# Optimization experiments

Hardware: AMD Instinct MI355X
Metric: run time of the kernel (lower is better)

The kernel has to match this reference:

```python
import jax, jax.numpy as jnp
import numpy as np

N, E, H, C, G = 20000, 320000, 6, 64, 64
NFEAT, EDGE_DIM = 6, 1
HC = H * C  # 384


def gat_conv(x, src, dst, ea, W, a_src, a_dst, W_e, a_e, b):
    """PyG GATConv (concat=True, negative_slope=0.2), self-loops already added.
    x:[N,in], src/dst:[E'], ea:[E',edge_dim]. Returns [N,H*C]."""
    n = x.shape[0]
    h = (x @ W.T).reshape(n, H, C)                       # [N,H,C]
    a_s = (h * a_src).sum(-1)                            # [N,H]
    a_d = (h * a_dst).sum(-1)                            # [N,H]
    e = (ea @ W_e.T).reshape(-1, H, C)                   # [E',H,C]
    a_ed = (e * a_e).sum(-1)                             # [E',H]
    alpha = jax.nn.leaky_relu(a_s[src] + a_d[dst] + a_ed, 0.2)
    # segment softmax over incoming edges of each dst node (stable)
    m = jax.ops.segment_max(alpha, dst, num_segments=n)  # every node has a self-loop
    ex = jnp.exp(alpha - m[dst])
    den = jax.ops.segment_sum(ex, dst, num_segments=n)
    att = ex / den[dst]                                  # [E',H]
    msg = h[src] * att[:, :, None]                       # [E',H,C]
    out = jax.ops.segment_sum(msg, dst, num_segments=n)
    return out.reshape(n, HC) + b


def add_self_loops(edge_index, edge_attr, n):
    loops = jnp.arange(n, dtype=edge_index.dtype)
    src = jnp.concatenate([edge_index[0], loops])
    dst = jnp.concatenate([edge_index[1], loops])
    fill = jnp.broadcast_to(edge_attr.mean(0, keepdims=True), (n, edge_attr.shape[1]))
    ea = jnp.concatenate([edge_attr, fill], axis=0)
    return src, dst, ea


def setup_inputs() -> dict:
    key = jax.random.key(0)
    ks = jax.random.split(key, 20)
    glorot = lambda k, shape: jax.random.normal(k, shape, jnp.float32) * np.sqrt(2.0 / (shape[-1] + shape[0]))
    inp = {
        "x": jax.random.normal(ks[0], (N, NFEAT), jnp.float32),
        "edge_attr": jax.random.uniform(ks[1], (E, EDGE_DIM), jnp.float32),
        "edge_index": jax.random.randint(ks[2], (2, E), 0, N, jnp.int64),
        "batch": jnp.sort(jax.random.randint(ks[3], (N,), 0, G, jnp.int64)),
        # conv1 params
        "w1": glorot(ks[4], (HC, NFEAT)),
        "att_src1": glorot(ks[5], (1, H, C)),
        "att_dst1": glorot(ks[6], (1, H, C)),
        "we1": glorot(ks[7], (HC, EDGE_DIM)),
        "atte1": glorot(ks[8], (1, H, C)),
        "b1": jnp.zeros((HC,), jnp.float32),
        # conv2 params
        "w2": glorot(ks[9], (HC, HC)),
        "att_src2": glorot(ks[10], (1, H, C)),
        "att_dst2": glorot(ks[11], (1, H, C)),
        "we2": glorot(ks[12], (HC, EDGE_DIM)),
        "atte2": glorot(ks[13], (1, H, C)),
        "b2": jnp.zeros((HC,), jnp.float32),
        # final linear (no bias)
        "w_lin": glorot(ks[14], (1, HC)),
    }
    return inp


def reference(x, edge_attr, w1, att_src1, att_dst1, we1, atte1, b1,
              w2, att_src2, att_dst2, we2, atte2, b2, w_lin,
              edge_index, batch):
    src, dst, ea = add_self_loops(edge_index, edge_attr, N)
    x1 = gat_conv(x, src, dst, ea, w1, att_src1, att_dst1, we1, atte1, b1)
    x2 = jax.nn.elu(x1)
    x3 = gat_conv(x2, src, dst, ea, w2, att_src2, att_dst2, we2, atte2, b2)
    x4 = jax.nn.elu(x3)
    # global mean pool over graphs
    sums = jax.ops.segment_sum(x4, batch, num_segments=G)
    cnt = jax.ops.segment_sum(jnp.ones((N, 1), x4.dtype), batch, num_segments=G)
    x5 = sums / jnp.maximum(cnt, 1.0)
    # dropout is identity in eval mode
    x7 = x5 @ w_lin.T
    return jax.nn.sigmoid(x7)
```

## Files before the change

### kernel.cpp

```cpp
#include <hip/hip_runtime.h>
#include <hip/hip_bf16.h>

constexpr int Nn  = 20000;
constexpr int Ee  = 320000;
constexpr int Hh  = 6;
constexpr int HC  = 384;
constexpr int Gg  = 64;
constexpr int NF  = 6;
constexpr int EP  = Ee + Nn;
constexpr int HW  = HC / 2;

typedef __attribute__((ext_vector_type(8))) short short8;
typedef __attribute__((ext_vector_type(4))) float f32x4;

constexpr size_t ALN(size_t x) { return (x + 255) & ~(size_t)255; }
constexpr size_t OFF_H1BF = 0;
constexpr size_t OFF_X2BF = ALN(OFF_H1BF + (size_t)Nn*HW*4);
constexpr size_t OFF_ATT  = ALN(OFF_X2BF + (size_t)Nn*HW*4);
constexpr size_t OFF_AS1  = ALN(OFF_ATT  + (size_t)EP*Hh*4);
constexpr size_t OFF_AD1  = ALN(OFF_AS1  + (size_t)Nn*Hh*4);
constexpr size_t OFF_AS2  = ALN(OFF_AD1  + (size_t)Nn*Hh*4);
constexpr size_t OFF_AD2  = ALN(OFF_AS2  + (size_t)Nn*Hh*4);
constexpr size_t OFF_OFFS = ALN(OFF_AD2  + (size_t)Nn*Hh*4);
constexpr size_t OFF_ESRC = ALN(OFF_OFFS + (size_t)(Nn+1)*4);
constexpr size_t OFF_EEA  = ALN(OFF_ESRC + (size_t)EP*4);
constexpr size_t OFF_W2BF = ALN(OFF_EEA  + (size_t)EP*4);
constexpr size_t OFF_ZERO = ALN(OFF_W2BF + (size_t)HC*HC*2);
constexpr size_t OFF_CNT  = OFF_ZERO;
constexpr size_t OFF_CNT2 = OFF_CNT  + (size_t)Nn*4;
constexpr size_t OFF_CNTG = OFF_CNT2 + (size_t)Nn*4;
constexpr size_t OFF_POOL = OFF_CNTG + (size_t)Gg*4;
constexpr size_t OFF_SCAL = OFF_POOL + (size_t)Gg*HC*4;
constexpr size_t ZERO_BYTES = OFF_SCAL + 64*4 - OFF_ZERO;

__device__ __forceinline__ float wave_red64(float v) {
    #pragma unroll
    for (int o = 32; o; o >>= 1) v += __shfl_down(v, o);
    return v;
}
__device__ __forceinline__ unsigned short f2bf(float f) {
    union { float f; unsigned u; } v; v.f = f;
    return (unsigned short)((v.u + 0x7fffu + ((v.u >> 16) & 1u)) >> 16);
}
__device__ __forceinline__ unsigned pack2(float a, float b) {
    return (unsigned)f2bf(a) | ((unsigned)f2bf(b) << 16);
}
__device__ __forceinline__ float blo(unsigned w) { union { unsigned u; float f; } v; v.u = w << 16; return v.f; }
__device__ __forceinline__ float bhi(unsigned w) { union { unsigned u; float f; } v; v.u = w & 0xffff0000u; return v.f; }

__global__ void k_mean(const float* __restrict__ ea, float* __restrict__ scal) {
    int i = blockIdx.x * blockDim.x + threadIdx.x;
    float v = 0.f;
    for (int j = i; j < Ee; j += gridDim.x * blockDim.x) v += ea[j];
    v = wave_red64(v);
    if ((threadIdx.x & 63) == 0) atomicAdd(&scal[0], v);
}

__global__ void k_wedot(const float* __restrict__ we1, const float* __restrict__ atte1,
                        const float* __restrict__ we2, const float* __restrict__ atte2,
                        float* __restrict__ scal) {
    int t = threadIdx.x;
    float p1 = we1[t] * atte1[t];
    float p2 = we2[t] * atte2[t];
    p1 = wave_red64(p1);
    p2 = wave_red64(p2);
    if ((t & 63) == 0) { int h = t >> 6; scal[1 + h] = p1; scal[7 + h] = p2; }
}

__global__ void k_cvtw(const float* __restrict__ w2, unsigned short* __restrict__ w2bf) {
    int i = blockIdx.x * blockDim.x + threadIdx.x;
    if (i < HC * HC) w2bf[i] = f2bf(w2[i]);
}

__global__ __launch_bounds__(HW) void k_h1(const float* __restrict__ x, const float* __restrict__ w1,
                                           const float* __restrict__ asrc, const float* __restrict__ adst,
                                           unsigned* __restrict__ h1bf, float* __restrict__ as_, float* __restrict__ ad_) {
    int n = blockIdx.x, t = threadIdx.x;
    int c0 = 2 * t, c1 = c0 + 1;
    float xv[NF];
    #pragma unroll
    for (int k = 0; k < NF; k++) xv[k] = x[n * NF + k];
    float a0 = 0.f, a1 = 0.f;
    #pragma unroll
    for (int k = 0; k < NF; k++) { a0 += xv[k] * w1[c0 * NF + k]; a1 += xv[k] * w1[c1 * NF + k]; }
    h1bf[(size_t)n * HW + t] = pack2(a0, a1);
    float s = a0 * asrc[c0] + a1 * asrc[c1];
    float d = a0 * adst[c0] + a1 * adst[c1];
    #pragma unroll
    for (int o = 16; o; o >>= 1) { s += __shfl_xor(s, o); d += __shfl_xor(d, o); }
    if ((t & 31) == 0) { int h = t >> 5; as_[n * Hh + h] = s; ad_[n * Hh + h] = d; }
}

__global__ void k_count(const int* __restrict__ dst, int* __restrict__ cnt) {
    int i = blockIdx.x * blockDim.x + threadIdx.x;
    if (i < EP) {
        int d = (i < Ee) ? dst[i] : (i - Ee);
        atomicAdd(&cnt[d], 1);
    }
}

__global__ __launch_bounds__(1024) void k_scan(const int* __restrict__ cnt, int* __restrict__ offs) {
    __shared__ int wsum[16];
    __shared__ int carry_s;
    int t = threadIdx.x, lane = t & 63, wid = t >> 6;
    if (t == 0) carry_s = 0;
    __syncthreads();
    for (int base = 0; base < Nn; base += 1024) {
        int idx = base + t;
        int v = (idx < Nn) ? cnt[idx] : 0;
        int x = v;
        #pragma unroll
        for (int o = 1; o < 64; o <<= 1) { int y = __shfl_up(x, o); if (lane >= o) x += y; }
        if (lane == 63) wsum[wid] = x;
        __syncthreads();
        int wbase = 0;
        for (int i = 0; i < wid; i++) wbase += wsum[i];
        int excl = carry_s + wbase + x - v;
        if (idx < Nn) offs[idx] = excl;
        __syncthreads();
        if (t == 1023) carry_s = excl + v;
        __syncthreads();
    }
    if (t == 0) offs[Nn] = carry_s;
}

__global__ void k_scatter(const int* __restrict__ src, const int* __restrict__ dst,
                          const float* __restrict__ ea, const int* __restrict__ offs,
                          int* __restrict__ cnt2, int* __restrict__ esrc, float* __restrict__ eea,
                          const float* __restrict__ scal) {
    int i = blockIdx.x * blockDim.x + threadIdx.x;
    if (i >= EP) return;
    int d, s; float a;
    if (i < Ee) { d = dst[i]; s = src[i]; a = ea[i]; }
    else        { d = i - Ee; s = d; a = scal[0] * (1.0f / Ee); }
    int p = offs[d] + atomicAdd(&cnt2[d], 1);
    esrc[p] = s;
    eea[p]  = a;
}

template <int LAYER>
__global__ void k_att(const float* __restrict__ as_, const float* __restrict__ ad_,
                      const int* __restrict__ offs, const int* __restrict__ esrc,
                      const float* __restrict__ eea, const float* __restrict__ scal,
                      float* __restrict__ att) {
    int idx = blockIdx.x * blockDim.x + threadIdx.x;
    if (idx >= Nn * Hh) return;
    int n = idx / Hh, h = idx - n * Hh;
    int s0 = offs[n], s1 = offs[n + 1];
    float adn = ad_[idx];
    float wdh = scal[(LAYER == 1 ? 1 : 7) + h];
    float m = -3.4e38f, den = 0.f;
    for (int j = s0; j < s1; ++j) {
        int s = esrc[j]; float a = eea[j];
        float al = as_[s * Hh + h] + adn + a * wdh;
        al = (al > 0.f) ? al : 0.2f * al;
        float mn = fmaxf(m, al);
        den = den * __expf(m - mn) + __expf(al - mn);
        m = mn;
    }
    float rden = 1.f / den;
    for (int j = s0; j < s1; ++j) {
        int s = esrc[j]; float a = eea[j];
        float al = as_[s * Hh + h] + adn + a * wdh;
        al = (al > 0.f) ? al : 0.2f * al;
        att[j * Hh + h] = __expf(al - m) * rden;
    }
}

template <int LAYER>
__global__ __launch_bounds__(HW) void k_agg(const unsigned* __restrict__ hbf, const float* __restrict__ att,
                                            const int* __restrict__ offs, const int* __restrict__ esrc,
                                            const float* __restrict__ bias, const int* __restrict__ batch,
                                            unsigned* __restrict__ xout, float* __restrict__ pool) {
    int n = blockIdx.x, t = threadIdx.x, h = t >> 5;
    int s0 = offs[n], s1 = offs[n + 1];
    float ax = 0.f, ay = 0.f;
    unsigned wA = 0; float aA = 0.f;
    int sB = 0;
    if (s0 < s1) {
        int sA = esrc[s0];
        wA = hbf[(size_t)sA * HW + t];
        aA = att[s0 * Hh + h];
        if (s0 + 1 < s1) sB = esrc[s0 + 1];
    }
    for (int j = s0; j < s1; ++j) {
        unsigned wB = 0; float aB = 0.f;
        int sC = sB;
        if (j + 2 < s1) sC = esrc[j + 2];
        if (j + 1 < s1) { wB = hbf[(size_t)sB * HW + t]; aB = att[(j + 1) * Hh + h]; }
        ax += aA * blo(wA);
        ay += aA * bhi(wA);
        wA = wB; aA = aB; sB = sC;
    }
    float o0 = ax + bias[2 * t], o1 = ay + bias[2 * t + 1];
    o0 = (o0 > 0.f) ? o0 : (__expf(o0) - 1.f);
    o1 = (o1 > 0.f) ? o1 : (__expf(o1) - 1.f);
    if (LAYER == 1) {
        xout[(size_t)n * HW + t] = pack2(o0, o1);
    } else {
        float* pp = pool + batch[n] * HC + 2 * t;
        atomicAdd(pp, o0);
        atomicAdd(pp + 1, o1);
    }
}

__global__ __launch_bounds__(256) void k_gemm(const unsigned short* __restrict__ x2bf,
                                              const unsigned short* __restrict__ w2bf,
                                              unsigned short* __restrict__ h2bf) {
    int t = threadIdx.x, l = t & 63, w = t >> 6;
    int m0 = blockIdx.x * 32;
    int n0 = w * 96;
    int lr = l & 15, lk = l >> 4;
    f32x4 acc[2][6];
    #pragma unroll
    for (int mi = 0; mi < 2; mi++)
        #pragma unroll
        for (int f = 0; f < 6; f++) acc[mi][f] = (f32x4){0.f, 0.f, 0.f, 0.f};
    int mrow0 = m0 + lr, mrow1 = m0 + 16 + lr;
    int r0 = mrow0 < Nn ? mrow0 : Nn - 1;
    int r1 = mrow1 < Nn ? mrow1 : Nn - 1;
    for (int ks = 0; ks < HC / 32; ks++) {
        int koff = ks * 32 + lk * 8;
        short8 a0 = *(const short8*)(x2bf + (size_t)r0 * HC + koff);
        short8 a1 = *(const short8*)(x2bf + (size_t)r1 * HC + koff);
        #pragma unroll
        for (int f = 0; f < 6; f++) {
            short8 b = *(const short8*)(w2bf + (size_t)(n0 + f * 16 + lr) * HC + koff);
            acc[0][f] = __builtin_amdgcn_mfma_f32_16x16x32_bf16(a0, b, acc[0][f], 0, 0, 0);
            acc[1][f] = __builtin_amdgcn_mfma_f32_16x16x32_bf16(a1, b, acc[1][f], 0, 0, 0);
        }
    }
    #pragma unroll
    for (int mi = 0; mi < 2; mi++) {
        int rowb = m0 + mi * 16 + lk * 4;
        #pragma unroll
        for (int r = 0; r < 4; r++) {
            int row = rowb + r;
            if (row < Nn) {
                unsigned short* dp = h2bf + (size_t)row * HC + n0 + lr;
                #pragma unroll
                for (int f = 0; f < 6; f++) dp[f * 16] = f2bf(acc[mi][f][r]);
            }
        }
    }
}

__global__ __launch_bounds__(HW) void k_attn2(const unsigned* __restrict__ h2bf, const float* __restrict__ asrc,
                                              const float* __restrict__ adst,
                                              float* __restrict__ as_, float* __restrict__ ad_) {
    int n = blockIdx.x, t = threadIdx.x;
    unsigned w = h2bf[(size_t)n * HW + t];
    float v0 = blo(w), v1 = bhi(w);
    float s = v0 * asrc[2 * t] + v1 * asrc[2 * t + 1];
    float d = v0 * adst[2 * t] + v1 * adst[2 * t + 1];
    #pragma unroll
    for (int o = 16; o; o >>= 1) { s += __shfl_xor(s, o); d += __shfl_xor(d, o); }
    if ((t & 31) == 0) { int h = t >> 5; as_[n * Hh + h] = s; ad_[n * Hh + h] = d; }
}

__global__ void k_cntg(const int* __restrict__ batch, int* __restrict__ cntg) {
    int i = blockIdx.x * blockDim.x + threadIdx.x;
    if (i < Nn) atomicAdd(&cntg[batch[i]], 1);
}

__global__ __launch_bounds__(HC) void k_final(const float* __restrict__ pool, const int* __restrict__ cntg,
                                              const float* __restrict__ wlin, float* __restrict__ out) {
    __shared__ float partial[Hh];
    int g = blockIdx.x, t = threadIdx.x;
    float v = pool[g * HC + t] * wlin[t];
    v = wave_red64(v);
    if ((t & 63) == 0) partial[t >> 6] = v;
    __syncthreads();
    if (t == 0) {
        float s = 0.f;
        #pragma unroll
        for (int h = 0; h < Hh; h++) s += partial[h];
        int c = cntg[g];
        float denom = (float)(c > 1 ? c : 1);
        out[g] = 1.f / (1.f + __expf(-s / denom));
    }
}

extern "C" void kernel_launch(void* const* d_in, const int* in_sizes, int n_in,
                              void* d_out, int out_size, void* d_ws, size_t ws_size,
                              hipStream_t stream) {
    const float* x        = (const float*)d_in[0];
    const float* ea       = (const float*)d_in[1];
    const int*   eidx     = (const int*)d_in[2];
    const int*   batch    = (const int*)d_in[3];
    const float* w1       = (const float*)d_in[4];
    const float* att_src1 = (const float*)d_in[5];
    const float* att_dst1 = (const float*)d_in[6];
    const float* we1      = (const float*)d_in[7];
    const float* atte1    = (const float*)d_in[8];
    const float* b1       = (const float*)d_in[9];
    const float* w2       = (const float*)d_in[10];
    const float* att_src2 = (const float*)d_in[11];
    const float* att_dst2 = (const float*)d_in[12];
    const float* we2      = (const float*)d_in[13];
    const float* atte2    = (const float*)d_in[14];
    const float* b2       = (const float*)d_in[15];
    const float* wlin     = (const float*)d_in[16];
    float* out = (float*)d_out;

    char* ws = (char*)d_ws;
    unsigned* h1bf = (unsigned*)(ws + OFF_H1BF);
    unsigned* x2bf = (unsigned*)(ws + OFF_X2BF);
    float* att  = (float*)(ws + OFF_ATT);
    float* as1  = (float*)(ws + OFF_AS1);
    float* ad1  = (float*)(ws + OFF_AD1);
    float* as2  = (float*)(ws + OFF_AS2);
    float* ad2  = (float*)(ws + OFF_AD2);
    int*   offs = (int*)(ws + OFF_OFFS);
    int*   esrc = (int*)(ws + OFF_ESRC);
    float* eea  = (float*)(ws + OFF_EEA);
    unsigned short* w2bf = (unsigned short*)(ws + OFF_W2BF);
    int*   cnt  = (int*)(ws + OFF_CNT);
    int*   cnt2 = (int*)(ws + OFF_CNT2);
    int*   cntg = (int*)(ws + OFF_CNTG);
    float* pool = (float*)(ws + OFF_POOL);
    float* scal = (float*)(ws + OFF_SCAL);

    const int* src = eidx;
    const int* dst = eidx + Ee;

    hipMemsetAsync(ws + OFF_ZERO, 0, ZERO_BYTES, stream);

    k_mean<<<256, 256, 0, stream>>>(ea, scal);
    k_wedot<<<1, HC, 0, stream>>>(we1, atte1, we2, atte2, scal);
    k_cvtw<<<(HC * HC + 255) / 256, 256, 0, stream>>>(w2, w2bf);

    k_h1<<<Nn, HW, 0, stream>>>(x, w1, att_src1, att_dst1, h1bf, as1, ad1);

    int ecb = (EP + 255) / 256;
    k_count<<<ecb, 256, 0, stream>>>(dst, cnt);
    k_scan<<<1, 1024, 0, stream>>>(cnt, offs);
    k_scatter<<<ecb, 256, 0, stream>>>(src, dst, ea, offs, cnt2, esrc, eea, scal);

    int nhb = (Nn * Hh + 255) / 256;
    k_att<1><<<nhb, 256, 0, stream>>>(as1, ad1, offs, esrc, eea, scal, att);
    k_agg<1><<<Nn, HW, 0, stream>>>(h1bf, att, offs, esrc, b1, nullptr, x2bf, nullptr);

    k_gemm<<<(Nn + 31) / 32, 256, 0, stream>>>((const unsigned short*)x2bf, w2bf, (unsigned short*)h1bf);
    k_attn2<<<Nn, HW, 0, stream>>>(h1bf, att_src2, att_dst2, as2, ad2);

    k_cntg<<<(Nn + 255) / 256, 256, 0, stream>>>(batch, cntg);

    k_att<2><<<nhb, 256, 0, stream>>>(as2, ad2, offs, esrc, eea, scal, att);
    k_agg<2><<<Nn, HW, 0, stream>>>(h1bf, att, offs, esrc, b2, batch, nullptr, pool);

    k_final<<<Gg, HC, 0, stream>>>(pool, cntg, wlin, out);
}
```

Baseline: 549.5 us.

## Restructure GAT attention and aggregation kernels, fuse small prep kernels

The attention kernel stops recomputing logits in a second pass. It stores leaky-relu logits in the att buffer, then exponentiates them in place, and writes the unnormalized softmax denominator to a new buffer. The aggregation kernel now handles two nodes per 192-thread block, loads 4 bf16 values per thread with uint2, unrolls edges by 4 with independent accumulators, and applies the 1/den normalization at the end. The small weight-convert and graph-count kernels are folded into the mean and edge-count kernels to cut launches. The cost is an extra read-modify-write pass over att in global memory.

```diff
diff --git a/kernel.cpp b/kernel.cpp
--- a/kernel.cpp
+++ b/kernel.cpp
@@ -17,7 +17,8 @@
 constexpr size_t OFF_H1BF = 0;
 constexpr size_t OFF_X2BF = ALN(OFF_H1BF + (size_t)Nn*HW*4);
 constexpr size_t OFF_ATT  = ALN(OFF_X2BF + (size_t)Nn*HW*4);
-constexpr size_t OFF_AS1  = ALN(OFF_ATT  + (size_t)EP*Hh*4);
+constexpr size_t OFF_DEN  = ALN(OFF_ATT  + (size_t)EP*Hh*4);
+constexpr size_t OFF_AS1  = ALN(OFF_DEN  + (size_t)Nn*Hh*4);
 constexpr size_t OFF_AD1  = ALN(OFF_AS1  + (size_t)Nn*Hh*4);
 constexpr size_t OFF_AS2  = ALN(OFF_AD1  + (size_t)Nn*Hh*4);
 constexpr size_t OFF_AD2  = ALN(OFF_AS2  + (size_t)Nn*Hh*4);
@@ -48,12 +49,15 @@
 __device__ __forceinline__ float blo(unsigned w) { union { unsigned u; float f; } v; v.u = w << 16; return v.f; }
 __device__ __forceinline__ float bhi(unsigned w) { union { unsigned u; float f; } v; v.u = w & 0xffff0000u; return v.f; }
 
-__global__ void k_mean(const float* __restrict__ ea, float* __restrict__ scal) {
+__global__ void k_prep(const float* __restrict__ ea, float* __restrict__ scal,
+                       const float* __restrict__ w2, unsigned short* __restrict__ w2bf) {
     int i = blockIdx.x * blockDim.x + threadIdx.x;
+    int stride = gridDim.x * blockDim.x;
     float v = 0.f;
-    for (int j = i; j < Ee; j += gridDim.x * blockDim.x) v += ea[j];
+    for (int j = i; j < Ee; j += stride) v += ea[j];
     v = wave_red64(v);
     if ((threadIdx.x & 63) == 0) atomicAdd(&scal[0], v);
+    for (int j = i; j < HC * HC; j += stride) w2bf[j] = f2bf(w2[j]);
 }
 
 __global__ void k_wedot(const float* __restrict__ we1, const float* __restrict__ atte1,
@@ -67,11 +71,6 @@
     if ((t & 63) == 0) { int h = t >> 6; scal[1 + h] = p1; scal[7 + h] = p2; }
 }
 
-__global__ void k_cvtw(const float* __restrict__ w2, unsigned short* __restrict__ w2bf) {
-    int i = blockIdx.x * blockDim.x + threadIdx.x;
-    if (i < HC * HC) w2bf[i] = f2bf(w2[i]);
-}
-
 __global__ __launch_bounds__(HW) void k_h1(const float* __restrict__ x, const float* __restrict__ w1,
                                            const float* __restrict__ asrc, const float* __restrict__ adst,
                                            unsigned* __restrict__ h1bf, float* __restrict__ as_, float* __restrict__ ad_) {
@@ -91,12 +90,14 @@
     if ((t & 31) == 0) { int h = t >> 5; as_[n * Hh + h] = s; ad_[n * Hh + h] = d; }
 }
 
-__global__ void k_count(const int* __restrict__ dst, int* __restrict__ cnt) {
+__global__ void k_count(const int* __restrict__ dst, int* __restrict__ cnt,
+                        const int* __restrict__ batch, int* __restrict__ cntg) {
     int i = blockIdx.x * blockDim.x + threadIdx.x;
     if (i < EP) {
         int d = (i < Ee) ? dst[i] : (i - Ee);
         atomicAdd(&cnt[d], 1);
     }
+    if (i < Nn) atomicAdd(&cntg[batch[i]], 1);
 }
 
 __global__ __launch_bounds__(1024) void k_scan(const int* __restrict__ cnt, int* __restrict__ offs) {
@@ -142,65 +143,99 @@
 __global__ void k_att(const float* __restrict__ as_, const float* __restrict__ ad_,
                       const int* __restrict__ offs, const int* __restrict__ esrc,
                       const float* __restrict__ eea, const float* __restrict__ scal,
-                      float* __restrict__ att) {
+                      float* __restrict__ att, float* __restrict__ den_out) {
     int idx = blockIdx.x * blockDim.x + threadIdx.x;
     if (idx >= Nn * Hh) return;
     int n = idx / Hh, h = idx - n * Hh;
     int s0 = offs[n], s1 = offs[n + 1];
     float adn = ad_[idx];
     float wdh = scal[(LAYER == 1 ? 1 : 7) + h];
-    float m = -3.4e38f, den = 0.f;
-    for (int j = s0; j < s1; ++j) {
-        int s = esrc[j]; float a = eea[j];
-        float al = as_[s * Hh + h] + adn + a * wdh;
+    float m = -3.4e38f;
+    int j = s0;
+    for (; j + 3 < s1; j += 4) {
+        int sa = esrc[j], sb = esrc[j+1], sc = esrc[j+2], sd = esrc[j+3];
+        float ea0 = eea[j], ea1 = eea[j+1], ea2 = eea[j+2], ea3 = eea[j+3];
+        float va = as_[sa * Hh + h];
+        float vb = as_[sb * Hh + h];
+        float vc = as_[sc * Hh + h];
+        float vd = as_[sd * Hh + h];
+        float A = va + adn + ea0 * wdh; A = (A > 0.f) ? A : 0.2f * A;
+        float B = vb + adn + ea1 * wdh; B = (B > 0.f) ? B : 0.2f * B;
+        float C = vc + adn + ea2 * wdh; C = (C > 0.f) ? C : 0.2f * C;
+        float D = vd + adn + ea3 * wdh; D = (D > 0.f) ? D : 0.2f * D;
+        att[j * Hh + h] = A; att[(j+1) * Hh + h] = B;
+        att[(j+2) * Hh + h] = C; att[(j+3) * Hh + h] = D;
+        m = fmaxf(m, fmaxf(fmaxf(A, B), fmaxf(C, D)));
+    }
+    for (; j < s1; ++j) {
+        int s = esrc[j];
+        float al = as_[s * Hh + h] + adn + eea[j] * wdh;
         al = (al > 0.f) ? al : 0.2f * al;
-        float mn = fmaxf(m, al);
-        den = den * __expf(m - mn) + __expf(al - mn);
-        m = mn;
-    }
-    float rden = 1.f / den;
-    for (int j = s0; j < s1; ++j) {
-        int s = esrc[j]; float a = eea[j];
-        float al = as_[s * Hh + h] + adn + a * wdh;
-        al = (al > 0.f) ? al : 0.2f * al;
-        att[j * Hh + h] = __expf(al - m) * rden;
-    }
+        att[j * Hh + h] = al;
+        m = fmaxf(m, al);
+    }
+    float den = 0.f;
+    for (j = s0; j < s1; ++j) {
+        float e = __expf(att[j * Hh + h] - m);
+        att[j * Hh + h] = e;
+        den += e;
+    }
+    den_out[idx] = den;
 }
 
 template <int LAYER>
-__global__ __launch_bounds__(HW) void k_agg(const unsigned* __restrict__ hbf, const float* __restrict__ att,
-                                            const int* __restrict__ offs, const int* __restrict__ esrc,
-                                            const float* __restrict__ bias, const int* __restrict__ batch,
-                                            unsigned* __restrict__ xout, float* __restrict__ pool) {
-    int n = blockIdx.x, t = threadIdx.x, h = t >> 5;
+__global__ __launch_bounds__(192) void k_agg(const uint2* __restrict__ hbf2, const float* __restrict__ att,
+                                             const float* __restrict__ den, const int* __restrict__ offs,
+                                             const int* __restrict__ esrc, const float* __restrict__ bias,
+                                             const int* __restrict__ batch,
+                                             uint2* __restrict__ xout, float* __restrict__ pool) {
+    int t = threadIdx.x;
+    int sub = t / 96, tt = t - sub * 96;
+    int n = blockIdx.x * 2 + sub;
+    int h = tt >> 4;
     int s0 = offs[n], s1 = offs[n + 1];
-    float ax = 0.f, ay = 0.f;
-    unsigned wA = 0; float aA = 0.f;
-    int sB = 0;
-    if (s0 < s1) {
-        int sA = esrc[s0];
-        wA = hbf[(size_t)sA * HW + t];
-        aA = att[s0 * Hh + h];
-        if (s0 + 1 < s1) sB = esrc[s0 + 1];
-    }
-    for (int j = s0; j < s1; ++j) {
-        unsigned wB = 0; float aB = 0.f;
-        int sC = sB;
-        if (j + 2 < s1) sC = esrc[j + 2];
-        if (j + 1 < s1) { wB = hbf[(size_t)sB * HW + t]; aB = att[(j + 1) * Hh + h]; }
-        ax += aA * blo(wA);
-        ay += aA * bhi(wA);
-        wA = wB; aA = aB; sB = sC;
-    }
-    float o0 = ax + bias[2 * t], o1 = ay + bias[2 * t + 1];
+    float x0a=0.f,x1a=0.f,x2a=0.f,x3a=0.f;
+    float x0b=0.f,x1b=0.f,x2b=0.f,x3b=0.f;
+    float x0c=0.f,x1c=0.f,x2c=0.f,x3c=0.f;
+    float x0d=0.f,x1d=0.f,x2d=0.f,x3d=0.f;
+    int j = s0;
+    for (; j + 3 < s1; j += 4) {
+        int sa = esrc[j], sb = esrc[j+1], sc = esrc[j+2], sd = esrc[j+3];
+        uint2 wa = hbf2[(size_t)sa * 96 + tt];
+        uint2 wb = hbf2[(size_t)sb * 96 + tt];
+        uint2 wc = hbf2[(size_t)sc * 96 + tt];
+        uint2 wd = hbf2[(size_t)sd * 96 + tt];
+        float fa = att[j * Hh + h], fb = att[(j+1) * Hh + h];
+        float fc = att[(j+2) * Hh + h], fd = att[(j+3) * Hh + h];
+        x0a += fa * blo(wa.x); x1a += fa * bhi(wa.x); x2a += fa * blo(wa.y); x3a += fa * bhi(wa.y);
+        x0b += fb * blo(wb.x); x1b += fb * bhi(wb.x); x2b += fb * blo(wb.y); x3b += fb * bhi(wb.y);
+        x0c += fc * blo(wc.x); x1c += fc * bhi(wc.x); x2c += fc * blo(wc.y); x3c += fc * bhi(wc.y);
+        x0d += fd * blo(wd.x); x1d += fd * bhi(wd.x); x2d += fd * blo(wd.y); x3d += fd * bhi(wd.y);
+    }
+    for (; j < s1; ++j) {
+        int s = esrc[j];
+        uint2 w = hbf2[(size_t)s * 96 + tt];
+        float f = att[j * Hh + h];
+        x0a += f * blo(w.x); x1a += f * bhi(w.x); x2a += f * blo(w.y); x3a += f * bhi(w.y);
+    }
+    float rden = 1.f / den[n * Hh + h];
+    int c0 = 4 * tt;
+    float o0 = (x0a + x0b + x0c + x0d) * rden + bias[c0];
+    float o1 = (x1a + x1b + x1c + x1d) * rden + bias[c0 + 1];
+    float o2 = (x2a + x2b + x2c + x2d) * rden + bias[c0 + 2];
+    float o3 = (x3a + x3b + x3c + x3d) * rden + bias[c0 + 3];
     o0 = (o0 > 0.f) ? o0 : (__expf(o0) - 1.f);
     o1 = (o1 > 0.f) ? o1 : (__expf(o1) - 1.f);
+    o2 = (o2 > 0.f) ? o2 : (__expf(o2) - 1.f);
+    o3 = (o3 > 0.f) ? o3 : (__expf(o3) - 1.f);
     if (LAYER == 1) {
-        xout[(size_t)n * HW + t] = pack2(o0, o1);
+        xout[(size_t)n * 96 + tt] = make_uint2(pack2(o0, o1), pack2(o2, o3));
     } else {
-        float* pp = pool + batch[n] * HC + 2 * t;
-        atomicAdd(pp, o0);
+        float* pp = pool + batch[n] * HC + c0;
+        atomicAdd(pp,     o0);
         atomicAdd(pp + 1, o1);
+        atomicAdd(pp + 2, o2);
+        atomicAdd(pp + 3, o3);
     }
 }
 
@@ -256,11 +291,6 @@
     #pragma unroll
     for (int o = 16; o; o >>= 1) { s += __shfl_xor(s, o); d += __shfl_xor(d, o); }
     if ((t & 31) == 0) { int h = t >> 5; as_[n * Hh + h] = s; ad_[n * Hh + h] = d; }
-}
-
-__global__ void k_cntg(const int* __restrict__ batch, int* __restrict__ cntg) {
-    int i = blockIdx.x * blockDim.x + threadIdx.x;
-    if (i < Nn) atomicAdd(&cntg[batch[i]], 1);
 }
 
 __global__ __launch_bounds__(HC) void k_final(const float* __restrict__ pool, const int* __restrict__ cntg,
@@ -307,6 +337,7 @@
     unsigned* h1bf = (unsigned*)(ws + OFF_H1BF);
     unsigned* x2bf = (unsigned*)(ws + OFF_X2BF);
     float* att  = (float*)(ws + OFF_ATT);
+    float* den  = (float*)(ws + OFF_DEN);
     float* as1  = (float*)(ws + OFF_AS1);
     float* ad1  = (float*)(ws + OFF_AD1);
     float* as2  = (float*)(ws + OFF_AS2);
@@ -326,28 +357,27 @@
 
     hipMemsetAsync(ws + OFF_ZERO, 0, ZERO_BYTES, stream);
 
-    k_mean<<<256, 256, 0, stream>>>(ea, scal);
+    k_prep<<<256, 256, 0, stream>>>(ea, scal, w2, w2bf);
     k_wedot<<<1, HC, 0, stream>>>(we1, atte1, we2, atte2, scal);
-    k_cvtw<<<(HC * HC + 255) / 256, 256, 0, stream>>>(w2, w2bf);
 
     k_h1<<<Nn, HW, 0, stream>>>(x, w1, att_src1, att_dst1, h1bf, as1, ad1);
 
     int ecb = (EP + 255) / 256;
-    k_count<<<ecb, 256, 0, stream>>>(dst, cnt);
+    k_count<<<ecb, 256, 0, stream>>>(dst, cnt, batch, cntg);
     k_scan<<<1, 1024, 0, stream>>>(cnt, offs);
     k_scatter<<<ecb, 256, 0, stream>>>(src, dst, ea, offs, cnt2, esrc, eea, scal);
 
     int nhb = (Nn * Hh + 255) / 256;
-    k_att<1><<<nhb, 256, 0, stream>>>(as1, ad1, offs, esrc, eea, scal, att);
-    k_agg<1><<<Nn, HW, 0, stream>>>(h1bf, att, offs, esrc, b1, nullptr, x2bf, nullptr);
+    k_att<1><<<nhb, 256, 0, stream>>>(as1, ad1, offs, esrc, eea, scal, att, den);
+    k_agg<1><<<Nn / 2, 192, 0, stream>>>((const uint2*)h1bf, att, den, offs, esrc, b1, nullptr,
+                                         (uint2*)x2bf, nullptr);
 
     k_gemm<<<(Nn + 31) / 32, 256, 0, stream>>>((const unsigned short*)x2bf, w2bf, (unsigned short*)h1bf);
     k_attn2<<<Nn, HW, 0, stream>>>(h1bf, att_src2, att_dst2, as2, ad2);
 
-    k_cntg<<<(Nn + 255) / 256, 256, 0, stream>>>(batch, cntg);
-
-    k_att<2><<<nhb, 256, 0, stream>>>(as2, ad2, offs, esrc, eea, scal, att);
-    k_agg<2><<<Nn, HW, 0, stream>>>(h1bf, att, offs, esrc, b2, batch, nullptr, pool);
+    k_att<2><<<nhb, 256, 0, stream>>>(as2, ad2, offs, esrc, eea, scal, att, den);
+    k_agg<2><<<Nn / 2, 192, 0, stream>>>((const uint2*)h1bf, att, den, offs, esrc, b2, batch,
+                                         nullptr, pool);
 
     k_final<<<Gg, HC, 0, stream>>>(pool, cntg, wlin, out);
 }
```

Result: slower. 579.5 us (+5.5%).
